# Optimization experiments

Hardware: AMD Instinct MI355X
Metric: run time of the kernel (lower is better)

The kernel has to match this reference:

```python
import jax, jax.numpy as jnp
import numpy as np

B, N, C, H = 32, 129, 768, 12
HID = 4 * C
EPS = 1e-5
NEG = -65504.0


def _layer_norm(x, g, b):
    mu = jnp.mean(x, axis=-1, keepdims=True)
    var = jnp.mean((x - mu) ** 2, axis=-1, keepdims=True)
    return (x - mu) / jnp.sqrt(var + EPS) * g + b


def _attn(x, m, g, b, wqkv, wproj):
    # x: [B, Nn, C], m: [B, Nn, 1] binary float mask
    Bb, Nn, Cc = x.shape
    hd = Cc // H
    xm = _layer_norm(x, g, b) * m
    qkv = (xm @ wqkv).reshape(Bb, Nn, 3, H, hd)
    q, k, v = (jnp.swapaxes(qkv[:, :, i], 1, 2) for i in range(3))  # [B,H,Nn,hd]
    att = jnp.einsum('bhqd,bhkd->bhqk', q, k) * (hd ** -0.5)
    outer = (m @ jnp.swapaxes(m, -1, -2))[:, None]  # [B,1,Nn,Nn] mask outer product
    att = jnp.where(outer == 0.0, NEG, att)
    att = jax.nn.softmax(att, axis=-1) * m[:, None]  # zero masked query rows
    out = jnp.einsum('bhqk,bhkd->bhqd', att, v)
    out = jnp.swapaxes(out, 1, 2).reshape(Bb, Nn, Cc)
    return out @ wproj


def _mlp(x, m, g, b, w1, w2):
    xm = _layer_norm(x, g, b) * m
    return jax.nn.gelu(xm @ w1, approximate=False) @ w2


def setup_inputs() -> dict:
    key = jax.random.key(0)
    ks = jax.random.split(key, 10)
    std = 0.02
    return {
        'RGB': jax.random.normal(ks[0], (B, N, C), jnp.float32),
        'NIR': jax.random.normal(ks[1], (B, N, C), jnp.float32),
        'TIR': jax.random.normal(ks[2], (B, N, C), jnp.float32),
        'mask': (jax.random.uniform(ks[3], (B, N - 1, 1)) > 0.3).astype(jnp.float32),
        'label': jax.random.randint(ks[4], (B,), 0, 171),
        # stacked params for branches [R, N, T, concat]
        'ln_g1': jnp.ones((4, C), jnp.float32),
        'ln_b1': jnp.zeros((4, C), jnp.float32),
        'w_qkv': std * jax.random.normal(ks[5], (4, C, 3 * C), jnp.float32),
        'w_proj': std * jax.random.normal(ks[6], (4, C, C), jnp.float32),
        'ln_g2': jnp.ones((4, C), jnp.float32),
        'ln_b2': jnp.zeros((4, C), jnp.float32),
        'w_fc1': std * jax.random.normal(ks[7], (4, C, HID), jnp.float32),
        'w_fc2': std * jax.random.normal(ks[8], (4, HID, C), jnp.float32),
        'out_g': jnp.ones((C,), jnp.float32),
        'out_b': jnp.zeros((C,), jnp.float32),
    }


def reference(RGB, NIR, TIR, mask, label, ln_g1, ln_b1, w_qkv, w_proj,
              ln_g2, ln_b2, w_fc1, w_fc2, out_g, out_b):
    m = jnp.concatenate([jnp.ones((RGB.shape[0], 1, 1), RGB.dtype), mask], axis=1)  # [B,N,1]

    def branch(x, i, mm):
        x = x + _attn(x, mm, ln_g1[i], ln_b1[i], w_qkv[i], w_proj[i])
        x = x + _mlp(x, mm, ln_g2[i], ln_b2[i], w_fc1[i], w_fc2[i])
        return x

    RGB = branch(RGB, 0, m)
    NIR = branch(NIR, 1, m)
    TIR = branch(TIR, 2, m)
    x = jnp.concatenate([RGB, NIR, TIR], axis=1)  # [B, 3N, C]
    m3 = jnp.tile(m, (1, 3, 1))
    x = branch(x, 3, m3)
    x = _layer_norm(x, out_g, out_b) * m3
    return x
```

## Files before the change

### kernel.cpp

```cpp
#include <hip/hip_runtime.h>

typedef unsigned short u16;
typedef __attribute__((ext_vector_type(4))) float f32x4;
typedef __attribute__((ext_vector_type(8))) short s16x8;
typedef __attribute__((ext_vector_type(4))) short s16x4;
typedef __attribute__((ext_vector_type(4))) unsigned short u16x4;

#define HH 12
#define CC 768
#define AS1(p) ((const __attribute__((address_space(1))) void*)(p))
#define AS3(p) ((__attribute__((address_space(3))) void*)(p))

__device__ inline u16 f2bf(float x){
  unsigned u = __float_as_uint(x);
  u = (u + 0x7FFFu + ((u >> 16) & 1u)) >> 16;
  return (u16)u;
}

__device__ inline f32x4 mfma32(s16x8 a, s16x8 b, f32x4 c){
  return __builtin_amdgcn_mfma_f32_16x16x32_bf16(a, b, c, 0, 0, 0);
}
__device__ inline f32x4 mfma16(s16x4 a, s16x4 b, f32x4 c){
  return __builtin_amdgcn_mfma_f32_16x16x16bf16_1k(a, b, c, 0, 0, 0);
}

__global__ void wtrans(const float* __restrict__ W, u16* __restrict__ Wt, int K, int N){
  __shared__ float tile[32][33];
  int k0 = blockIdx.x*32, n0 = blockIdx.y*32;
  const float* Wz = W + (size_t)blockIdx.z*K*N;
  u16* Wtz = Wt + (size_t)blockIdx.z*K*N;
  int tx = threadIdx.x & 31, ty = threadIdx.x >> 5;
  #pragma unroll
  for(int r = ty; r < 32; r += 8)
    tile[r][tx] = Wz[(size_t)(k0+r)*N + n0 + tx];
  __syncthreads();
  #pragma unroll
  for(int r = ty; r < 32; r += 8)
    Wtz[(size_t)(n0+r)*K + k0 + tx] = f2bf(tile[tx][r]);
}

__global__ void initcat(const float* __restrict__ R, const float* __restrict__ Nr,
                        const float* __restrict__ T, float* __restrict__ xcat){
  int idx = blockIdx.x*256 + threadIdx.x;
  const int per = 32*129*768/4;
  if(idx >= per) return;
  int z = blockIdx.y;
  const float* src = z == 0 ? R : (z == 1 ? Nr : T);
  float4 v = ((const float4*)src)[idx];
  int e = idx*4;
  int row = e / 768, c = e - row*768;
  int bb2 = row / 129, nn = row - bb2*129;
  ((float4*)xcat)[((size_t)(bb2*387 + z*129 + nn)*768 + c)/4] = v;
}

__device__ inline float maskval(const float* m, int b, int n){
  return (n == 0) ? 1.0f : m[b*128 + n - 1];
}

template<int F32OUT>
__global__ __launch_bounds__(64) void ln_mask(
    const float* __restrict__ x,
    const float* __restrict__ gg, const float* __restrict__ bb, int zsG,
    const float* __restrict__ mask,
    void* __restrict__ out, size_t zsO,
    int tpb, int zoffmul)
{
  int r = blockIdx.x, z = blockIdx.y, lane = threadIdx.x;
  int bidx = r / tpb, nn = r - bidx*tpb;
  size_t cat = (size_t)bidx*387 + z*zoffmul + nn;
  const float4* xr = (const float4*)(x + cat*CC);
  float4 v[3]; float s = 0.f, sq = 0.f;
  #pragma unroll
  for(int w = 0; w < 3; ++w){
    v[w] = xr[w*64 + lane];
    s  += v[w].x + v[w].y + v[w].z + v[w].w;
    sq += v[w].x*v[w].x + v[w].y*v[w].y + v[w].z*v[w].z + v[w].w*v[w].w;
  }
  #pragma unroll
  for(int o = 32; o; o >>= 1){ s += __shfl_xor(s, o); sq += __shfl_xor(sq, o); }
  float mu = s * (1.f/768.f);
  float var = sq * (1.f/768.f) - mu*mu;
  float rstd = rsqrtf(var + 1e-5f);
  float mv = maskval(mask, bidx, nn % 129);
  const float4* g4 = (const float4*)(gg + (size_t)z*zsG);
  const float4* b4 = (const float4*)(bb + (size_t)z*zsG);
  #pragma unroll
  for(int w = 0; w < 3; ++w){
    float4 gv = g4[w*64+lane], bv = b4[w*64+lane];
    float y0 = ((v[w].x - mu)*rstd*gv.x + bv.x) * mv;
    float y1 = ((v[w].y - mu)*rstd*gv.y + bv.y) * mv;
    float y2 = ((v[w].z - mu)*rstd*gv.z + bv.z) * mv;
    float y3 = ((v[w].w - mu)*rstd*gv.w + bv.w) * mv;
    if(F32OUT){
      ((float4*)out)[cat*(CC/4) + w*64 + lane] = make_float4(y0,y1,y2,y3);
    } else {
      u16x4 p; p.x = f2bf(y0); p.y = f2bf(y1); p.z = f2bf(y2); p.w = f2bf(y3);
      ((u16x4*)((u16*)out + z*zsO + (size_t)r*CC))[w*64 + lane] = p;
    }
  }
}

template<int EPI, int TPB>
__global__ __launch_bounds__(256) void gemm_bt(
    const u16* __restrict__ A, size_t zsA,
    const u16* __restrict__ Bt, size_t zsB,
    void* __restrict__ O, size_t zsO,
    int M, int N, int K,
    int zoffmul)
{
  __shared__ u16 As[2][4096];
  __shared__ u16 Bs[2][4096];
  int z = blockIdx.z;
  const u16* Az = A + zsA*(size_t)z;
  const u16* Bz = Bt + zsB*(size_t)z;

  int gx = gridDim.x, gy = gridDim.y;
  int nwg = gx*gy;
  int orig = blockIdx.x + gx*blockIdx.y;
  int q = nwg >> 3, r8 = nwg & 7;
  int xcd = orig & 7, off = orig >> 3;
  int wg = (xcd < r8 ? xcd*(q+1) : r8*(q+1) + (xcd-r8)*q) + off;
  int bx = wg / gy, by = wg - bx*gy;
  int m0 = bx*128, n0 = by*128;

  int tid = threadIdx.x, wid = tid >> 6, lane = tid & 63;
  int wr = wid >> 1, wc = wid & 1;
  int lrow = lane & 15, g4 = lane >> 4, lk8 = g4*8;

  int e0 = wid*512 + lane*8;
  int row0 = e0 >> 5, col0 = e0 & 31;
  int ra0 = m0 + row0;      ra0 = ra0 < M ? ra0 : M - 1;
  int ra1 = m0 + row0 + 64; ra1 = ra1 < M ? ra1 : M - 1;
  const u16* pa0 = Az + (size_t)ra0*K + col0;
  const u16* pa1 = Az + (size_t)ra1*K + col0;
  const u16* pb0 = Bz + (size_t)(n0 + row0)*K + col0;
  const u16* pb1 = Bz + (size_t)(n0 + row0 + 64)*K + col0;
  int lofs = wid*512;

  __builtin_amdgcn_global_load_lds(AS1(pa0), AS3(&As[0][lofs]),        16, 0, 0);
  __builtin_amdgcn_global_load_lds(AS1(pa1), AS3(&As[0][lofs + 2048]), 16, 0, 0);
  __builtin_amdgcn_global_load_lds(AS1(pb0), AS3(&Bs[0][lofs]),        16, 0, 0);
  __builtin_amdgcn_global_load_lds(AS1(pb1), AS3(&Bs[0][lofs + 2048]), 16, 0, 0);
  pa0 += 32; pa1 += 32; pb0 += 32; pb1 += 32;
  __syncthreads();

  f32x4 acc[4][4] = {};
  int NT = K >> 5;
  int cur = 0;

  for(int t = 0; t < NT; ++t){
    if(t + 1 < NT){
      int nxt = cur ^ 1;
      __builtin_amdgcn_global_load_lds(AS1(pa0), AS3(&As[nxt][lofs]),        16, 0, 0);
      __builtin_amdgcn_global_load_lds(AS1(pa1), AS3(&As[nxt][lofs + 2048]), 16, 0, 0);
      __builtin_amdgcn_global_load_lds(AS1(pb0), AS3(&Bs[nxt][lofs]),        16, 0, 0);
      __builtin_amdgcn_global_load_lds(AS1(pb1), AS3(&Bs[nxt][lofs + 2048]), 16, 0, 0);
      pa0 += 32; pa1 += 32; pb0 += 32; pb1 += 32;
    }
    s16x8 aF[4], bF[4];
    #pragma unroll
    for(int i = 0; i < 4; ++i){
      aF[i] = *(const s16x8*)&As[cur][(wr*64 + i*16 + lrow)*32 + lk8];
      bF[i] = *(const s16x8*)&Bs[cur][(wc*64 + i*16 + lrow)*32 + lk8];
    }
    #pragma unroll
    for(int i = 0; i < 4; ++i)
      #pragma unroll
      for(int jn = 0; jn < 4; ++jn)
        acc[i][jn] = mfma32(aF[i], bF[jn], acc[i][jn]);
    __syncthreads();
    cur ^= 1;
  }

  u16* Oz = (u16*)O + zsO*(size_t)z;
  int zb = z*zoffmul;
  #pragma unroll
  for(int i = 0; i < 4; ++i){
    #pragma unroll
    for(int r = 0; r < 4; ++r){
      int row = m0 + wr*64 + i*16 + g4*4 + r;
      if(row >= M) continue;
      #pragma unroll
      for(int jn = 0; jn < 4; ++jn){
        int col = n0 + wc*64 + jn*16 + lrow;
        float v = acc[i][jn][r];
        if constexpr (EPI == 0){
          Oz[(size_t)row*N + col] = f2bf(v);
        } else if constexpr (EPI == 1){
          float u = v*(0.7978845608f + 0.0356774081f*v*v);
          float t = 1.f - 2.f/(__expf(2.f*u) + 1.f);
          Oz[(size_t)row*N + col] = f2bf(0.5f*v*(1.f + t));
        } else {
          int bi = row / TPB, nnn = row - bi*TPB;
          size_t cat = (size_t)bi*387 + zb + nnn;
          float* dst = (float*)O + cat*CC + col;
          *dst += v;
        }
      }
    }
  }
}

template<int N_>
__global__ __launch_bounds__(256) void attn3(
    const u16* __restrict__ qkv, size_t zsQ,
    u16* __restrict__ out, size_t zsO,
    const float* __restrict__ mask)
{
  constexpr int NC  = (N_ + 63)/64;
  constexpr int NKC = NC*64;
  constexpr float SCL = 0.125f*1.44269504088896f;
  __shared__ u16 Ks[2][64][66];
  __shared__ u16 Vt[2][64][68];
  __shared__ float Msk[NKC];

  int z = blockIdx.z;
  int bh = blockIdx.y, b = bh / HH, hh = bh - b*HH;
  int tid = threadIdx.x, wid = tid >> 6, lane = tid & 63;
  int lq = lane & 15, g = lane >> 4;
  const u16* qz = qkv + zsQ*(size_t)z;
  const size_t rowbase = (size_t)b*N_;
  const u16* kbase = qz + rowbase*2304 + 768 + hh*64;
  const u16* vbase = kbase + 768;

  for(int k = tid; k < NKC; k += 256){
    float mk = 0.f;
    if(k < N_){ int nn = (N_ > 129) ? (k % 129) : k; mk = (nn == 0) ? 1.f : mask[b*128 + nn - 1]; }
    Msk[k] = (mk != 0.f) ? 0.f : -1e30f;
  }

  int q0 = blockIdx.x*64 + wid*16;
  int qrow = q0 + lq;
  int qrc = qrow < N_ ? qrow : N_ - 1;
  const u16* qptr = qz + (rowbase + qrc)*2304 + hh*64;
  s16x8 qF0 = *(const s16x8*)(qptr + g*8);
  s16x8 qF1 = *(const s16x8*)(qptr + 32 + g*8);

  int r0 = tid >> 3, c16 = tid & 7;
  s16x8 kr[2], vr[2];
  const s16x8 zv = {0,0,0,0,0,0,0,0};

  #pragma unroll
  for(int i = 0; i < 2; ++i){
    int row = r0 + i*32;
    kr[i] = (row < N_) ? *(const s16x8*)(kbase + (size_t)row*2304 + c16*8) : zv;
    vr[i] = (row < N_) ? *(const s16x8*)(vbase + (size_t)row*2304 + c16*8) : zv;
  }
  #pragma unroll
  for(int i = 0; i < 2; ++i){
    *(s16x8*)&Ks[0][r0 + i*32][c16*8] = kr[i];
    #pragma unroll
    for(int j = 0; j < 8; ++j) Vt[0][c16*8 + j][r0 + i*32] = (u16)vr[i][j];
  }
  __syncthreads();

  f32x4 o[4] = {};
  float l = 0.f;

  for(int ch = 0; ch < NC; ++ch){
    int cur = ch & 1;
    if(ch + 1 < NC){
      #pragma unroll
      for(int i = 0; i < 2; ++i){
        int row = (ch + 1)*64 + r0 + i*32;
        kr[i] = (row < N_) ? *(const s16x8*)(kbase + (size_t)row*2304 + c16*8) : zv;
        vr[i] = (row < N_) ? *(const s16x8*)(vbase + (size_t)row*2304 + c16*8) : zv;
      }
    }
    float pT[4][4];
    #pragma unroll
    for(int t = 0; t < 4; ++t){
      s16x8 kF0 = *(const s16x8*)&Ks[cur][t*16 + lq][g*8];
      s16x8 kF1 = *(const s16x8*)&Ks[cur][t*16 + lq][32 + g*8];
      f32x4 s = {0.f,0.f,0.f,0.f};
      s = mfma32(kF0, qF0, s);
      s = mfma32(kF1, qF1, s);
      const float* mrow = &Msk[ch*64 + t*16 + g*4];
      #pragma unroll
      for(int r = 0; r < 4; ++r){
        float p = exp2f(fmaf(s[r], SCL, mrow[r]));
        pT[t][r] = p;
        l += p;
      }
    }
    #pragma unroll
    for(int t = 0; t < 4; ++t){
      s16x4 pa;
      #pragma unroll
      for(int r = 0; r < 4; ++r) pa[r] = (short)f2bf(pT[t][r]);
      #pragma unroll
      for(int db = 0; db < 4; ++db){
        s16x4 vf = *(const s16x4*)&Vt[cur][db*16 + lq][t*16 + g*4];
        o[db] = mfma16(pa, vf, o[db]);
      }
    }
    if(ch + 1 < NC){
      int nxt = (ch + 1) & 1;
      #pragma unroll
      for(int i = 0; i < 2; ++i){
        *(s16x8*)&Ks[nxt][r0 + i*32][c16*8] = kr[i];
        #pragma unroll
        for(int j = 0; j < 8; ++j) Vt[nxt][c16*8 + j][r0 + i*32] = (u16)vr[i][j];
      }
      __syncthreads();
    }
  }

  l += __shfl_xor(l, 16);
  l += __shfl_xor(l, 32);
  float mq = 0.f;
  if(qrow < N_) mq = (Msk[qrow] == 0.f) ? 1.f : 0.f;
  float sc = mq / l;
  float scr[4];
  #pragma unroll
  for(int r = 0; r < 4; ++r) scr[r] = __shfl(sc, g*4 + r);

  #pragma unroll
  for(int db = 0; db < 4; ++db){
    #pragma unroll
    for(int r = 0; r < 4; ++r){
      int qq = q0 + g*4 + r;
      if(qq < N_)
        out[zsO*(size_t)z + (rowbase + qq)*CC + hh*64 + db*16 + lq] = f2bf(o[db][r]*scr[r]);
    }
  }
}

extern "C" void kernel_launch(void* const* d_in, const int* in_sizes, int n_in,
                              void* d_out, int out_size, void* d_ws, size_t ws_size,
                              hipStream_t stream)
{
  const float* RGB   = (const float*)d_in[0];
  const float* NIR   = (const float*)d_in[1];
  const float* TIR   = (const float*)d_in[2];
  const float* mask  = (const float*)d_in[3];
  const float* ln_g1 = (const float*)d_in[5];
  const float* ln_b1 = (const float*)d_in[6];
  const float* w_qkv = (const float*)d_in[7];
  const float* w_proj= (const float*)d_in[8];
  const float* ln_g2 = (const float*)d_in[9];
  const float* ln_b2 = (const float*)d_in[10];
  const float* w_fc1 = (const float*)d_in[11];
  const float* w_fc2 = (const float*)d_in[12];
  const float* out_g = (const float*)d_in[13];
  const float* out_b = (const float*)d_in[14];

  char* p = (char*)d_ws;
  u16* wqkv_t  = (u16*)p; p += (size_t)4*2304*768*2;
  u16* wproj_t = (u16*)p; p += (size_t)4*768*768*2;
  u16* w1_t    = (u16*)p; p += (size_t)4*768*3072*2;
  u16* w2_t    = (u16*)p; p += (size_t)4*3072*768*2;
  float* xcat  = (float*)p; p += (size_t)12384*768*4;
  u16* xm      = (u16*)p; p += (size_t)3*4224*768*2;
  u16* qkv     = (u16*)p; p += (size_t)3*4224*3072*2;
  u16* hbuf    = qkv;
  if((size_t)(p - (char*)d_ws) > ws_size) return;

  wtrans<<<dim3(24, 72, 4), 256, 0, stream>>>(w_qkv, wqkv_t, 768, 2304);
  wtrans<<<dim3(24, 24, 4), 256, 0, stream>>>(w_proj, wproj_t, 768, 768);
  wtrans<<<dim3(24, 96, 4), 256, 0, stream>>>(w_fc1, w1_t, 768, 3072);
  wtrans<<<dim3(96, 24, 4), 256, 0, stream>>>(w_fc2, w2_t, 3072, 768);
  initcat<<<dim3(3096, 3), 256, 0, stream>>>(RGB, NIR, TIR, xcat);

  const int M3 = 4128;
  const size_t zxm = (size_t)4224*768, zqkv = (size_t)4224*2304, zh = (size_t)4224*3072;
  ln_mask<0><<<dim3(M3,3), 64, 0, stream>>>(xcat, ln_g1, ln_b1, 768, mask, xm, zxm, 129, 129);
  gemm_bt<0,1><<<dim3(33,18,3), 256, 0, stream>>>(xm, zxm, wqkv_t, (size_t)2304*768, qkv, zqkv, M3, 2304, 768, 0);
  attn3<129><<<dim3(3,384,3), 256, 0, stream>>>(qkv, zqkv, xm, zxm, mask);
  gemm_bt<2,129><<<dim3(33,6,3), 256, 0, stream>>>(xm, zxm, wproj_t, (size_t)768*768, xcat, 0, M3, 768, 768, 129);
  ln_mask<0><<<dim3(M3,3), 64, 0, stream>>>(xcat, ln_g2, ln_b2, 768, mask, xm, zxm, 129, 129);
  gemm_bt<1,1><<<dim3(33,24,3), 256, 0, stream>>>(xm, zxm, w1_t, (size_t)768*3072, hbuf, zh, M3, 3072, 768, 0);
  gemm_bt<2,129><<<dim3(33,6,3), 256, 0, stream>>>(hbuf, zh, w2_t, (size_t)768*3072, xcat, 0, M3, 768, 3072, 129);
  const int M1 = 12384;
  ln_mask<0><<<dim3(M1,1), 64, 0, stream>>>(xcat, ln_g1 + 3*768, ln_b1 + 3*768, 0, mask, xm, 0, 387, 0);
  gemm_bt<0,1><<<dim3(97,18,1), 256, 0, stream>>>(xm, 0, wqkv_t + (size_t)3*2304*768, 0, qkv, 0, M1, 2304, 768, 0);
  attn3<387><<<dim3(7,384,1), 256, 0, stream>>>(qkv, 0, xm, 0, mask);
  gemm_bt<2,387><<<dim3(97,6,1), 256, 0, stream>>>(xm, 0, wproj_t + (size_t)3*768*768, 0, xcat, 0, M1, 768, 768, 0);
  ln_mask<0><<<dim3(M1,1), 64, 0, stream>>>(xcat, ln_g2 + 3*768, ln_b2 + 3*768, 0, mask, xm, 0, 387, 0);
  gemm_bt<1,1><<<dim3(97,24,1), 256, 0, stream>>>(xm, 0, w1_t + (size_t)3*768*3072, 0, hbuf, 0, M1, 3072, 768, 0);
  gemm_bt<2,387><<<dim3(97,6,1), 256, 0, stream>>>(hbuf, 0, w2_t + (size_t)3*768*3072, 0, xcat, 0, M1, 768, 3072, 0);
  ln_mask<1><<<dim3(M1,1), 64, 0, stream>>>(xcat, out_g, out_b, 0, mask, d_out, 0, 387, 0);
}
```

Before: 810.8 us.

## Triple-buffer GEMM LDS tiles with explicit vmcnt waits and raw barriers

Changes the bf16 GEMM main loop from double to triple buffering, so two K-tiles of direct global-to-LDS loads are in flight ahead of the compute. Explicit s_waitcnt vmcnt counts wait only for the current tile, and raw s_barrier replaces __syncthreads. The aim is to hide global memory latency better. In exchange, LDS use per block rises from 32KB to 48KB, which may lower occupancy, and the hand-counted vmcnt values must stay in step with the number of loads issued per stage.

```diff
diff --git a/kernel.cpp b/kernel.cpp
--- a/kernel.cpp
+++ b/kernel.cpp
@@ -108,8 +108,8 @@
     int M, int N, int K,
     int zoffmul)
 {
-  __shared__ u16 As[2][4096];
-  __shared__ u16 Bs[2][4096];
+  __shared__ u16 As[3][4096];
+  __shared__ u16 Bs[3][4096];
   int z = blockIdx.z;
   const u16* Az = A + zsA*(size_t)z;
   const u16* Bz = Bt + zsB*(size_t)z;
@@ -137,26 +137,31 @@
   const u16* pb1 = Bz + (size_t)(n0 + row0 + 64)*K + col0;
   int lofs = wid*512;
 
-  __builtin_amdgcn_global_load_lds(AS1(pa0), AS3(&As[0][lofs]),        16, 0, 0);
-  __builtin_amdgcn_global_load_lds(AS1(pa1), AS3(&As[0][lofs + 2048]), 16, 0, 0);
-  __builtin_amdgcn_global_load_lds(AS1(pb0), AS3(&Bs[0][lofs]),        16, 0, 0);
-  __builtin_amdgcn_global_load_lds(AS1(pb1), AS3(&Bs[0][lofs + 2048]), 16, 0, 0);
-  pa0 += 32; pa1 += 32; pb0 += 32; pb1 += 32;
-  __syncthreads();
+  auto stage = [&](int b){
+    __builtin_amdgcn_global_load_lds(AS1(pa0), AS3(&As[b][lofs]),        16, 0, 0);
+    __builtin_amdgcn_global_load_lds(AS1(pa1), AS3(&As[b][lofs + 2048]), 16, 0, 0);
+    __builtin_amdgcn_global_load_lds(AS1(pb0), AS3(&Bs[b][lofs]),        16, 0, 0);
+    __builtin_amdgcn_global_load_lds(AS1(pb1), AS3(&Bs[b][lofs + 2048]), 16, 0, 0);
+    pa0 += 32; pa1 += 32; pb0 += 32; pb1 += 32;
+  };
+
+  int NT = K >> 5;
+  stage(0);
+  stage(1);
 
   f32x4 acc[4][4] = {};
-  int NT = K >> 5;
-  int cur = 0;
+  int cur = 0, nxt = 2;
 
   for(int t = 0; t < NT; ++t){
-    if(t + 1 < NT){
-      int nxt = cur ^ 1;
-      __builtin_amdgcn_global_load_lds(AS1(pa0), AS3(&As[nxt][lofs]),        16, 0, 0);
-      __builtin_amdgcn_global_load_lds(AS1(pa1), AS3(&As[nxt][lofs + 2048]), 16, 0, 0);
-      __builtin_amdgcn_global_load_lds(AS1(pb0), AS3(&Bs[nxt][lofs]),        16, 0, 0);
-      __builtin_amdgcn_global_load_lds(AS1(pb1), AS3(&Bs[nxt][lofs + 2048]), 16, 0, 0);
-      pa0 += 32; pa1 += 32; pb0 += 32; pb1 += 32;
-    }
+    if(t + 2 < NT){
+      stage(nxt);
+      asm volatile("s_waitcnt vmcnt(8)" ::: "memory");
+    } else if(t + 1 < NT){
+      asm volatile("s_waitcnt vmcnt(4)" ::: "memory");
+    } else {
+      asm volatile("s_waitcnt vmcnt(0)" ::: "memory");
+    }
+    __builtin_amdgcn_s_barrier();
     s16x8 aF[4], bF[4];
     #pragma unroll
     for(int i = 0; i < 4; ++i){
@@ -168,8 +173,9 @@
       #pragma unroll
       for(int jn = 0; jn < 4; ++jn)
         acc[i][jn] = mfma32(aF[i], bF[jn], acc[i][jn]);
-    __syncthreads();
-    cur ^= 1;
+    __builtin_amdgcn_s_barrier();
+    cur = (cur + 1 == 3) ? 0 : cur + 1;
+    nxt = (nxt + 1 == 3) ? 0 : nxt + 1;
   }
 
   u16* Oz = (u16*)O + zsO*(size_t)z;
```

After: 801.0 us. About the same (-1.2%).
